# Performance work log

Hardware: AMD Instinct MI355X
Metric: run time of the kernel (lower is better)

## Reference

```python
import jax, jax.numpy as jnp
import numpy as np
from jax import lax

B, T_ENCO, N_INP, N_HID, T_DECO = 1024, 128, 128, 256, 24


def _lin(x, W, b):
    return x @ W.T + b


def _lstm_cell(x, h, c, Wih, Whh, bih, bhh):
    # PyTorch LSTMCell gate order: input, forget, cell(g), output
    g = x @ Wih.T + bih + h @ Whh.T + bhh
    i, f, gg, o = jnp.split(g, 4, axis=-1)
    c2 = jax.nn.sigmoid(f) * c + jax.nn.sigmoid(i) * jnp.tanh(gg)
    return jax.nn.sigmoid(o) * jnp.tanh(c2), c2


def setup_inputs() -> dict:
    key = jax.random.key(0)
    ks = iter(jax.random.split(key, 48))
    def w(shape, s=0.05):
        return jax.random.normal(next(ks), shape, jnp.float32) * s
    m = N_HID
    return {
        "input_p_q": jax.random.normal(next(ks), (B, T_ENCO, N_INP), jnp.float32),
        "label_p": jax.random.normal(next(ks), (B, T_DECO), jnp.float32),
        "Ue_W": w((m, T_ENCO)), "Ue_b": w((m,)),
        "Ue2_W": w((m, N_INP)), "Ue2_b": w((m,)),
        "We_W": w((m, 2 * N_HID)), "We_b": w((m,)),
        "Ve_W": w((1, m)), "Ve_b": w((1,)),
        "Ud_W": w((N_HID, N_HID)), "Ud_b": w((N_HID,)),
        "Wd_W": w((N_HID, 2 * N_HID)), "Wd_b": w((N_HID,)),
        "Vd_W": w((1, N_HID)), "Vd_b": w((1,)),
        "enc_Wih": w((4 * N_HID, N_INP)), "enc_Whh": w((4 * N_HID, N_HID)),
        "enc_bih": w((4 * N_HID,)), "enc_bhh": w((4 * N_HID,)),
        "mid_Wih": w((4 * N_HID, N_HID)), "mid_Whh": w((4 * N_HID, N_HID)),
        "mid_bih": w((4 * N_HID,)), "mid_bhh": w((4 * N_HID,)),
        "dec_Wih": w((4 * N_HID, N_HID)), "dec_Whh": w((4 * N_HID, N_HID)),
        "dec_bih": w((4 * N_HID,)), "dec_bhh": w((4 * N_HID,)),
        "reg_W": w((1, N_HID)), "reg_b": w((1,)),
    }


def reference(input_p_q, label_p, Ue_W, Ue_b, Ue2_W, Ue2_b, We_W, We_b, Ve_W, Ve_b,
              Ud_W, Ud_b, Wd_W, Wd_b, Vd_W, Vd_b,
              enc_Wih, enc_Whh, enc_bih, enc_bhh,
              mid_Wih, mid_Whh, mid_bih, mid_bhh,
              dec_Wih, dec_Whh, dec_bih, dec_bhh,
              reg_W, reg_b):
    bsz = input_p_q.shape[0]
    inputs = input_p_q[:, :T_ENCO, :]                       # [B, T, n_inp]
    # Ue(inputs.transpose(1,2)) is loop-invariant: [B, n_inp, m]
    ue_x = _lin(jnp.swapaxes(inputs, 1, 2), Ue_W, Ue_b)
    z = jnp.zeros((bsz, N_HID), inputs.dtype)

    # --- spatial-attention encoder (LSTMCell over time) ---
    def enc_step(carry, x_i):                               # x_i: [B, n_inp]
        h, c = carry
        hc = _lin(jnp.concatenate([h, c], axis=1), We_W, We_b)[:, None, :]
        xi = _lin(x_i, Ue2_W, Ue2_b)[:, None, :]
        score = _lin(jnp.tanh(hc + ue_x + xi), Ve_W, Ve_b)[..., 0]  # [B, n_inp]
        a = jax.nn.softmax(score, axis=1)
        h2, c2 = _lstm_cell(x_i * a, h, c, enc_Wih, enc_Whh, enc_bih, enc_bhh)
        return (h2, c2), h2

    _, enc_hs = lax.scan(enc_step, (z, z), jnp.swapaxes(inputs, 0, 1))  # [T, B, H]

    # --- middle single-layer LSTM (zero init state) ---
    def mid_step(carry, x_t):
        h, c = carry
        h2, c2 = _lstm_cell(x_t, h, c, mid_Wih, mid_Whh, mid_bih, mid_bhh)
        return (h2, c2), h2

    _, mid = lax.scan(mid_step, (z, z), enc_hs)
    mid = jnp.swapaxes(mid, 0, 1)                            # [B, T, H]
    ud_mid = _lin(mid, Ud_W, Ud_b)                           # loop-invariant

    # --- temporal-attention decoder (note: raw (un-softmaxed) scores used in bmm,
    #     matching the original code) ---
    def dec_step(carry, _):
        hi, ci = carry
        wd = _lin(jnp.concatenate([hi, ci], axis=1), Wd_W, Wd_b)[:, None, :]
        t = _lin(jnp.tanh(wd + ud_mid), Vd_W, Vd_b)[..., 0]  # [B, T]
        dec_in = jnp.einsum('bt,bth->bh', t, mid)
        hi2, ci2 = _lstm_cell(dec_in, hi, ci, dec_Wih, dec_Whh, dec_bih, dec_bhh)
        return (hi2, ci2), hi2

    _, dec = lax.scan(dec_step, (z, z), None, length=T_DECO + 6)
    dec = jnp.swapaxes(dec, 0, 1)                            # [B, T_deco+6, H]
    out = _lin(dec, reg_W, reg_b)[..., 0]                    # [B, T_deco+6]
    return out[:, -T_DECO:]
```

## Files before the change

kernel.cpp:

```cpp
#include <hip/hip_runtime.h>


#define B_   1024
#define T_   128
#define NI_  128
#define H_   256
#define H4_  1024
#define TD_  24
#define DS_  30
#define BB   4
#define TB   1024

typedef _Float16 hf_t;
typedef _Float16 half8  __attribute__((ext_vector_type(8)));
typedef _Float16 half2v __attribute__((ext_vector_type(2)));

__device__ __forceinline__ float sigm(float x) {
    return __builtin_amdgcn_rcpf(1.0f + __expf(-x));
}
__device__ __forceinline__ float tanh_f(float x) {
    float e = __expf(2.0f * x);
    return 1.0f - 2.0f * __builtin_amdgcn_rcpf(e + 1.0f);
}
__device__ __forceinline__ float fdot2f(half2v a, half2v b, float c) {
#if __has_builtin(__builtin_amdgcn_fdot2)
    return __builtin_amdgcn_fdot2(a, b, c, false);
#else
    return fmaf((float)a.x, (float)b.x, fmaf((float)a.y, (float)b.y, c));
#endif
}
__device__ __forceinline__ float dot8h(half8 w, half8 x, float acc) {
    acc = fdot2f(__builtin_shufflevector(w, w, 0, 1), __builtin_shufflevector(x, x, 0, 1), acc);
    acc = fdot2f(__builtin_shufflevector(w, w, 2, 3), __builtin_shufflevector(x, x, 2, 3), acc);
    acc = fdot2f(__builtin_shufflevector(w, w, 4, 5), __builtin_shufflevector(x, x, 4, 5), acc);
    acc = fdot2f(__builtin_shufflevector(w, w, 6, 7), __builtin_shufflevector(x, x, 6, 7), acc);
    return acc;
}
__device__ __forceinline__ hf_t nt_load_h(const hf_t* p) {
#if __has_builtin(__builtin_nontemporal_load)
    return __builtin_nontemporal_load(p);
#else
    return *p;
#endif
}
__device__ __forceinline__ void nt_store_h(hf_t v, hf_t* p) {
#if __has_builtin(__builtin_nontemporal_store)
    __builtin_nontemporal_store(v, p);
#else
    *p = v;
#endif
}

#define W_WE    0u
#define W_UE2   131072u
#define W_EWIH  163840u
#define W_EWHH  294912u
#define W_MWIH  557056u
#define W_MWHH  819200u
#define W_DWIH  1081344u
#define W_DWHH  1343488u
#define W_WD    1605632u
#define W_UD    1736704u
#define SCR_A   2097152u
#define SCR_B   35651584u

__global__ void convw_kernel(const float* __restrict__ sWE, const float* __restrict__ sUE2,
                             const float* __restrict__ sEI, const float* __restrict__ sEH,
                             const float* __restrict__ sMI, const float* __restrict__ sMH,
                             const float* __restrict__ sDI, const float* __restrict__ sDH,
                             const float* __restrict__ sWD, const float* __restrict__ sUD,
                             hf_t* __restrict__ dst) {
    const int gtid = blockIdx.x * blockDim.x + threadIdx.x;
    const int gs   = gridDim.x * blockDim.x;
    for (int n = gtid; n < 131072; n += gs) {
        int e = n & 7, q = n >> 3, k = q & 255, c = q >> 8, kq = c >> 4, i = c & 15;
        dst[W_WE + n] = (hf_t)sWE[k * 512 + kq * 128 + i * 8 + e];
    }
    for (int n = gtid; n < 32768; n += gs) {
        int e = n & 7, q = n >> 3, k = q & 255, c = q >> 8, kq = c >> 2, i = c & 3;
        dst[W_UE2 + n] = (hf_t)sUE2[k * 128 + kq * 32 + i * 8 + e];
    }
    for (int n = gtid; n < 131072; n += gs) {
        int e = n & 7, q = n >> 3, o = q & 1023, i = q >> 10;
        dst[W_EWIH + n] = (hf_t)sEI[o * 128 + i * 8 + e];
    }
    for (int n = gtid; n < 262144; n += gs) {
        int e = n & 7, q = n >> 3, o = q & 1023, i = q >> 10;
        int s = o * 256 + i * 8 + e;
        dst[W_EWHH + n] = (hf_t)sEH[s];
        dst[W_MWIH + n] = (hf_t)sMI[s];
        dst[W_MWHH + n] = (hf_t)sMH[s];
        dst[W_DWIH + n] = (hf_t)sDI[s];
        dst[W_DWHH + n] = (hf_t)sDH[s];
    }
    for (int n = gtid; n < 131072; n += gs) {
        int e = n & 7, q = n >> 3, k = q & 255, c = q >> 8, kq = c >> 4, i = c & 15;
        dst[W_WD + n] = (hf_t)sWD[k * 512 + kq * 128 + i * 8 + e];
    }
    for (int n = gtid; n < 65536; n += gs)
        dst[W_UD + n] = (hf_t)sUD[n];
}

#define O_HC    0
#define O_CF    1024
#define O_HM    2048
#define O_CMF   2560
#define O_XRAW  3584
#define O_XH    4096
#define O_XG    4352
#define O_HCXI  4608
#define O_SPART 5632
#define O_SBUF  6656
#define O_GBUF  7168
#define O_DINH  11264
#define O_HF    11776
#define O_VES   12800
#define O_VDS   13056

__global__ __launch_bounds__(TB, 4) void dsrnn_kernel(
    const float* __restrict__ inp,
    const float* __restrict__ UeW,  const float* __restrict__ Ueb,
    const float* __restrict__ Ue2b,
    const float* __restrict__ Web,
    const float* __restrict__ VeW,  const float* __restrict__ Veb,
    const float* __restrict__ Udb,
    const float* __restrict__ Wdb,
    const float* __restrict__ VdW,  const float* __restrict__ Vdb,
    const float* __restrict__ ebih, const float* __restrict__ ebhh,
    const float* __restrict__ mbih, const float* __restrict__ mbhh,
    const float* __restrict__ dbih, const float* __restrict__ dbhh,
    const float* __restrict__ rW,   const float* __restrict__ rb,
    const hf_t* __restrict__ wb,
    hf_t* __restrict__ scrA,
    hf_t* __restrict__ scrB,
    float* __restrict__ out)
{
    __shared__ float sm[16384];
    const int tid = threadIdx.x;
    const int b0  = blockIdx.x * BB;

    hf_t*  hc   = (hf_t*)(sm + O_HC);
    float* cf   = sm + O_CF;
    hf_t*  hm   = (hf_t*)(sm + O_HM);
    float* cmf  = sm + O_CMF;
    float* xraw = sm + O_XRAW;
    hf_t*  xh   = (hf_t*)(sm + O_XH);
    hf_t*  xg   = (hf_t*)(sm + O_XG);
    float* hcxi = sm + O_HCXI;
    float* spart= sm + O_SPART;
    float* sbuf = sm + O_SBUF;
    float* gbuf = sm + O_GBUF;
    hf_t*  dinh = (hf_t*)(sm + O_DINH);
    float* hful = sm + O_HF;
    float* ves  = sm + O_VES;
    float* vds  = sm + O_VDS;

    {
        const int j = tid & 127, kq8 = tid >> 7;
        for (int b = 0; b < BB; ++b) {
            __syncthreads();
            const float* Xg = inp + (size_t)(b0 + b) * T_ * NI_;
            for (int i = tid; i < T_ * NI_; i += TB) sm[i] = Xg[i];
            __syncthreads();
            hf_t* ub = scrA + (size_t)(b0 + b) * H_ * NI_;
            for (int k = kq8 * 32; k < kq8 * 32 + 32; ++k) {
                const float* wrow = UeW + (size_t)k * T_;
                float acc = Ueb[k];
#pragma unroll 4
                for (int t = 0; t < T_; ++t) acc = fmaf(wrow[t], sm[t * NI_ + j], acc);
                nt_store_h((hf_t)acc, ub + (size_t)k * NI_ + j);
            }
        }
    }
    __syncthreads();
    for (int i = tid; i < 3584; i += TB) sm[i] = 0.0f;
    if (tid < 256) { ves[tid] = VeW[tid]; vds[tid] = VdW[tid]; }
    __syncthreads();

    for (int t = 0; t < T_; ++t) {
        if (tid < 512) {
            const int b = tid >> 7, j = tid & 127;
            float v = inp[((size_t)(b0 + b) * T_ + t) * NI_ + j];
            xraw[b * NI_ + j] = v;
            xh[b * NI_ + j]   = (hf_t)v;
        }
        __syncthreads();

        {
            const int k = tid & 255, kq = tid >> 8;
            const half8* wWE = (const half8*)(wb + W_WE)  + (size_t)(kq * 16) * 256 + k;
            const half8* wU2 = (const half8*)(wb + W_UE2) + (size_t)(kq * 4)  * 256 + k;
            float a0 = 0.f, a1 = 0.f, a2 = 0.f, a3 = 0.f;
#pragma unroll 8
            for (int i = 0; i < 16; ++i) {
                half8 w = wWE[(size_t)i * 256];
                a0 = dot8h(w, *(const half8*)&hc[0 * 512 + kq * 128 + i * 8], a0);
                a1 = dot8h(w, *(const half8*)&hc[1 * 512 + kq * 128 + i * 8], a1);
                a2 = dot8h(w, *(const half8*)&hc[2 * 512 + kq * 128 + i * 8], a2);
                a3 = dot8h(w, *(const half8*)&hc[3 * 512 + kq * 128 + i * 8], a3);
            }
#pragma unroll
            for (int i = 0; i < 4; ++i) {
                half8 w = wU2[(size_t)i * 256];
                a0 = dot8h(w, *(const half8*)&xh[0 * 128 + kq * 32 + i * 8], a0);
                a1 = dot8h(w, *(const half8*)&xh[1 * 128 + kq * 32 + i * 8], a1);
                a2 = dot8h(w, *(const half8*)&xh[2 * 128 + kq * 32 + i * 8], a2);
                a3 = dot8h(w, *(const half8*)&xh[3 * 128 + kq * 32 + i * 8], a3);
            }
            gbuf[kq * 1024 + 0 * 256 + k] = a0;
            gbuf[kq * 1024 + 1 * 256 + k] = a1;
            gbuf[kq * 1024 + 2 * 256 + k] = a2;
            gbuf[kq * 1024 + 3 * 256 + k] = a3;
        }
        __syncthreads();
        {
            const int b = tid >> 8, k = tid & 255;
            hcxi[b * 256 + k] = gbuf[b * 256 + k] + gbuf[1024 + b * 256 + k]
                              + gbuf[2048 + b * 256 + k] + gbuf[3072 + b * 256 + k]
                              + Web[k] + Ue2b[k];
        }
        __syncthreads();

        {
            const int b = tid >> 8, r = tid & 255, kh = r >> 7, j = r & 127;
            const hf_t* up = scrA + ((size_t)(b0 + b) * 256 + kh * 128) * 128 + j;
            const float* hx = hcxi + b * 256 + kh * 128;
            const float* vw = ves + kh * 128;
            float acc = kh ? 0.f : Veb[0];
#pragma unroll 8
            for (int k2 = 0; k2 < 128; ++k2) {
                float u = (float)nt_load_h(up + (size_t)k2 * 128);
                acc = fmaf(vw[k2], tanh_f(hx[k2] + u), acc);
            }
            spart[tid] = acc;
        }
        __syncthreads();

        if (tid < 256) {
            const int b = tid >> 6, lane = tid & 63;
            const int base = b << 8;
            float sA = spart[base + lane]      + spart[base + 128 + lane];
            float sB = spart[base + 64 + lane] + spart[base + 192 + lane];
            float m = fmaxf(sA, sB);
            for (int d = 1; d < 64; d <<= 1) m = fmaxf(m, __shfl_xor(m, d));
            float eA = __expf(sA - m), eB = __expf(sB - m);
            float ssum = eA + eB;
            for (int d = 1; d < 64; d <<= 1) ssum += __shfl_xor(ssum, d);
            float inv = 1.0f / ssum;
            xg[b * NI_ + lane]      = (hf_t)(xraw[b * NI_ + lane] * eA * inv);
            xg[b * NI_ + lane + 64] = (hf_t)(xraw[b * NI_ + lane + 64] * eB * inv);
        }
        __syncthreads();

        {
            const int o = tid;
            const half8* wih = (const half8*)(wb + W_EWIH) + o;
            const half8* whh = (const half8*)(wb + W_EWHH) + o;
            float bias = ebih[o] + ebhh[o];
            float a0 = bias, a1 = bias, a2 = bias, a3 = bias;
#pragma unroll 8
            for (int i = 0; i < 16; ++i) {
                half8 w = wih[(size_t)i * 1024];
                a0 = dot8h(w, *(const half8*)&xg[0 * 128 + i * 8], a0);
                a1 = dot8h(w, *(const half8*)&xg[1 * 128 + i * 8], a1);
                a2 = dot8h(w, *(const half8*)&xg[2 * 128 + i * 8], a2);
                a3 = dot8h(w, *(const half8*)&xg[3 * 128 + i * 8], a3);
            }
#pragma unroll 8
            for (int i = 0; i < 32; ++i) {
                half8 w = whh[(size_t)i * 1024];
                a0 = dot8h(w, *(const half8*)&hc[0 * 512 + i * 8], a0);
                a1 = dot8h(w, *(const half8*)&hc[1 * 512 + i * 8], a1);
                a2 = dot8h(w, *(const half8*)&hc[2 * 512 + i * 8], a2);
                a3 = dot8h(w, *(const half8*)&hc[3 * 512 + i * 8], a3);
            }
            gbuf[0 * 1024 + o] = a0; gbuf[1 * 1024 + o] = a1;
            gbuf[2 * 1024 + o] = a2; gbuf[3 * 1024 + o] = a3;
        }
        __syncthreads();

        {
            const int b = tid >> 8, k = tid & 255;
            float gi = gbuf[b * H4_ + k];
            float gf = gbuf[b * H4_ + H_ + k];
            float gg = gbuf[b * H4_ + 2 * H_ + k];
            float go = gbuf[b * H4_ + 3 * H_ + k];
            float c2 = sigm(gf) * cf[b * H_ + k] + sigm(gi) * tanh_f(gg);
            float h2 = sigm(go) * tanh_f(c2);
            cf[b * H_ + k] = c2;
            hc[b * 512 + k]       = (hf_t)h2;
            hc[b * 512 + 256 + k] = (hf_t)c2;
        }
        __syncthreads();

        {
            const int o = tid;
            const half8* wih = (const half8*)(wb + W_MWIH) + o;
            const half8* whh = (const half8*)(wb + W_MWHH) + o;
            float bias = mbih[o] + mbhh[o];
            float a0 = bias, a1 = bias, a2 = bias, a3 = bias;
#pragma unroll 8
            for (int i = 0; i < 32; ++i) {
                half8 w = wih[(size_t)i * 1024];
                a0 = dot8h(w, *(const half8*)&hc[0 * 512 + i * 8], a0);
                a1 = dot8h(w, *(const half8*)&hc[1 * 512 + i * 8], a1);
                a2 = dot8h(w, *(const half8*)&hc[2 * 512 + i * 8], a2);
                a3 = dot8h(w, *(const half8*)&hc[3 * 512 + i * 8], a3);
            }
#pragma unroll 8
            for (int i = 0; i < 32; ++i) {
                half8 w = whh[(size_t)i * 1024];
                a0 = dot8h(w, *(const half8*)&hm[0 * 256 + i * 8], a0);
                a1 = dot8h(w, *(const half8*)&hm[1 * 256 + i * 8], a1);
                a2 = dot8h(w, *(const half8*)&hm[2 * 256 + i * 8], a2);
                a3 = dot8h(w, *(const half8*)&hm[3 * 256 + i * 8], a3);
            }
            gbuf[0 * 1024 + o] = a0; gbuf[1 * 1024 + o] = a1;
            gbuf[2 * 1024 + o] = a2; gbuf[3 * 1024 + o] = a3;
        }
        __syncthreads();

        {
            const int b = tid >> 8, k = tid & 255;
            float gi = gbuf[b * H4_ + k];
            float gf = gbuf[b * H4_ + H_ + k];
            float gg = gbuf[b * H4_ + 2 * H_ + k];
            float go = gbuf[b * H4_ + 3 * H_ + k];
            float c2 = sigm(gf) * cmf[b * H_ + k] + sigm(gi) * tanh_f(gg);
            float h2 = sigm(go) * tanh_f(c2);
            cmf[b * H_ + k] = c2;
            hm[b * 256 + k] = (hf_t)h2;
            scrB[((size_t)(b0 + b) * T_ + t) * H_ + k] = (hf_t)h2;
        }
        __syncthreads();
    }

    {
        const int b = tid >> 8, r = tid & 255, oh = r >> 7, tt = r & 127;
        const half8* mrow = (const half8*)(scrB + ((size_t)(b0 + b) * T_ + tt) * H_);
        half8 m[32];
#pragma unroll
        for (int i = 0; i < 32; ++i) m[i] = mrow[i];
        const half8* udw = (const half8*)(wb + W_UD);
        for (int o2 = 0; o2 < 128; ++o2) {
            const int o = oh * 128 + o2;
            const half8* ur = udw + (size_t)o * 32;
            float acc = Udb[o];
#pragma unroll 8
            for (int i = 0; i < 32; ++i) acc = dot8h(ur[i], m[i], acc);
            nt_store_h((hf_t)acc, scrA + ((size_t)(b0 + b) * 256 + o) * 128 + tt);
        }
    }
    __syncthreads();
    for (int i = tid; i < 2048; i += TB) sm[i] = 0.0f;
    __syncthreads();

    for (int s = 0; s < DS_; ++s) {
        {
            const int k = tid & 255, kq = tid >> 8;
            const half8* wWD = (const half8*)(wb + W_WD) + (size_t)(kq * 16) * 256 + k;
            float a0 = 0.f, a1 = 0.f, a2 = 0.f, a3 = 0.f;
#pragma unroll 8
            for (int i = 0; i < 16; ++i) {
                half8 w = wWD[(size_t)i * 256];
                a0 = dot8h(w, *(const half8*)&hc[0 * 512 + kq * 128 + i * 8], a0);
                a1 = dot8h(w, *(const half8*)&hc[1 * 512 + kq * 128 + i * 8], a1);
                a2 = dot8h(w, *(const half8*)&hc[2 * 512 + kq * 128 + i * 8], a2);
                a3 = dot8h(w, *(const half8*)&hc[3 * 512 + kq * 128 + i * 8], a3);
            }
            gbuf[kq * 1024 + 0 * 256 + k] = a0;
            gbuf[kq * 1024 + 1 * 256 + k] = a1;
            gbuf[kq * 1024 + 2 * 256 + k] = a2;
            gbuf[kq * 1024 + 3 * 256 + k] = a3;
        }
        __syncthreads();
        {
            const int b = tid >> 8, k = tid & 255;
            hcxi[b * 256 + k] = gbuf[b * 256 + k] + gbuf[1024 + b * 256 + k]
                              + gbuf[2048 + b * 256 + k] + gbuf[3072 + b * 256 + k]
                              + Wdb[k];
        }
        __syncthreads();

        {
            const int b = tid >> 8, r = tid & 255, kh = r >> 7, j = r & 127;
            const hf_t* up = scrA + ((size_t)(b0 + b) * 256 + kh * 128) * 128 + j;
            const float* hx = hcxi + b * 256 + kh * 128;
            const float* vw = vds + kh * 128;
            float acc = kh ? 0.f : Vdb[0];
#pragma unroll 8
            for (int k2 = 0; k2 < 128; ++k2) {
                float u = (float)nt_load_h(up + (size_t)k2 * 128);
                acc = fmaf(vw[k2], tanh_f(hx[k2] + u), acc);
            }
            spart[tid] = acc;
        }
        __syncthreads();
        if (tid < 512) {
            const int b = tid >> 7, j = tid & 127;
            sbuf[b * T_ + j] = spart[(b << 8) + j] + spart[(b << 8) + 128 + j];
        }
        __syncthreads();

        {
            const int b = tid >> 8, h = tid & 255;
            const hf_t* mp = scrB + (size_t)(b0 + b) * T_ * H_ + h;
            float acc = 0.0f;
            for (int j = 0; j < T_; ++j)
                acc = fmaf(sbuf[b * T_ + j], (float)mp[(size_t)j * H_], acc);
            dinh[b * 256 + h] = (hf_t)acc;
        }
        __syncthreads();

        {
            const int o = tid;
            const half8* wih = (const half8*)(wb + W_DWIH) + o;
            const half8* whh = (const half8*)(wb + W_DWHH) + o;
            float bias = dbih[o] + dbhh[o];
            float a0 = bias, a1 = bias, a2 = bias, a3 = bias;
#pragma unroll 8
            for (int i = 0; i < 32; ++i) {
                half8 w = wih[(size_t)i * 1024];
                a0 = dot8h(w, *(const half8*)&dinh[0 * 256 + i * 8], a0);
                a1 = dot8h(w, *(const half8*)&dinh[1 * 256 + i * 8], a1);
                a2 = dot8h(w, *(const half8*)&dinh[2 * 256 + i * 8], a2);
                a3 = dot8h(w, *(const half8*)&dinh[3 * 256 + i * 8], a3);
            }
#pragma unroll 8
            for (int i = 0; i < 32; ++i) {
                half8 w = whh[(size_t)i * 1024];
                a0 = dot8h(w, *(const half8*)&hc[0 * 512 + i * 8], a0);
                a1 = dot8h(w, *(const half8*)&hc[1 * 512 + i * 8], a1);
                a2 = dot8h(w, *(const half8*)&hc[2 * 512 + i * 8], a2);
                a3 = dot8h(w, *(const half8*)&hc[3 * 512 + i * 8], a3);
            }
            gbuf[0 * 1024 + o] = a0; gbuf[1 * 1024 + o] = a1;
            gbuf[2 * 1024 + o] = a2; gbuf[3 * 1024 + o] = a3;
        }
        __syncthreads();

        {
            const int b = tid >> 8, k = tid & 255;
            float gi = gbuf[b * H4_ + k];
            float gf = gbuf[b * H4_ + H_ + k];
            float gg = gbuf[b * H4_ + 2 * H_ + k];
            float go = gbuf[b * H4_ + 3 * H_ + k];
            float c2 = sigm(gf) * cf[b * H_ + k] + sigm(gi) * tanh_f(gg);
            float h2 = sigm(go) * tanh_f(c2);
            cf[b * H_ + k] = c2;
            hc[b * 512 + k]       = (hf_t)h2;
            hc[b * 512 + 256 + k] = (hf_t)c2;
            hful[b * H_ + k] = h2;
        }
        __syncthreads();

        if (s >= 6 && tid < 256) {
            const int b = tid >> 6, lane = tid & 63;
            float p = rW[lane]       * hful[b * H_ + lane]
                    + rW[lane + 64]  * hful[b * H_ + lane + 64]
                    + rW[lane + 128] * hful[b * H_ + lane + 128]
                    + rW[lane + 192] * hful[b * H_ + lane + 192];
            for (int d = 1; d < 64; d <<= 1) p += __shfl_xor(p, d);
            if (lane == 0) out[(size_t)(b0 + b) * TD_ + (s - 6)] = p + rb[0];
        }
        __syncthreads();
    }
}

extern "C" void kernel_launch(void* const* d_in, const int* in_sizes, int n_in,
                              void* d_out, int out_size, void* d_ws, size_t ws_size,
                              hipStream_t stream) {
    const float* inp  = (const float*)d_in[0];
    const float* UeW  = (const float*)d_in[2];
    const float* Ueb  = (const float*)d_in[3];
    const float* Ue2W = (const float*)d_in[4];
    const float* Ue2b = (const float*)d_in[5];
    const float* WeW  = (const float*)d_in[6];
    const float* Web  = (const float*)d_in[7];
    const float* VeW  = (const float*)d_in[8];
    const float* Veb  = (const float*)d_in[9];
    const float* UdW  = (const float*)d_in[10];
    const float* Udb  = (const float*)d_in[11];
    const float* WdW  = (const float*)d_in[12];
    const float* Wdb  = (const float*)d_in[13];
    const float* VdW  = (const float*)d_in[14];
    const float* Vdb  = (const float*)d_in[15];
    const float* eWih = (const float*)d_in[16];
    const float* eWhh = (const float*)d_in[17];
    const float* ebih = (const float*)d_in[18];
    const float* ebhh = (const float*)d_in[19];
    const float* mWih = (const float*)d_in[20];
    const float* mWhh = (const float*)d_in[21];
    const float* mbih = (const float*)d_in[22];
    const float* mbhh = (const float*)d_in[23];
    const float* dWih = (const float*)d_in[24];
    const float* dWhh = (const float*)d_in[25];
    const float* dbih = (const float*)d_in[26];
    const float* dbhh = (const float*)d_in[27];
    const float* rW   = (const float*)d_in[28];
    const float* rb   = (const float*)d_in[29];

    hf_t* wsb  = (hf_t*)d_ws;
    hf_t* scrA = wsb + SCR_A;
    hf_t* scrB = wsb + SCR_B;

    convw_kernel<<<512, 256, 0, stream>>>(WeW, Ue2W, eWih, eWhh, mWih, mWhh,
                                          dWih, dWhh, WdW, UdW, wsb);

    dsrnn_kernel<<<B_ / BB, TB, 0, stream>>>(
        inp, UeW, Ueb, Ue2b, Web, VeW, Veb, Udb, Wdb, VdW, Vdb,
        ebih, ebhh, mbih, mbhh, dbih, dbhh, rW, rb,
        wsb, scrA, scrB, (float*)d_out);
}
```

Baseline: 10.75 ms.

## Keep half of the Ue/Ud attention projections resident in enlarged dynamic LDS

Switches to 160KB of dynamic shared memory and keeps the first 128 rows of the precomputed Ue(x) and Ud(mid) projections per batch element in LDS, so half of the per-step attention reads no longer go to global scratch. The working buffers are compacted and aliased. The LSTM cell states move into registers, and the regression dot product is reduced with a warp shuffle plus a small LDS reduce. In exchange, LDS use grows far beyond the old 64KB, which limits blocks per CU to one. The Ue precompute is also reorganised into two half-width passes with extra syncs.

```diff
diff --git a/kernel.cpp b/kernel.cpp
--- a/kernel.cpp
+++ b/kernel.cpp
@@ -10,6 +10,7 @@
 #define DS_  30
 #define BB   4
 #define TB   1024
+#define LDS_BYTES 163840u
 
 typedef _Float16 hf_t;
 typedef _Float16 half8  __attribute__((ext_vector_type(8)));
@@ -102,20 +103,14 @@
 }
 
 #define O_HC    0
-#define O_CF    1024
-#define O_HM    2048
-#define O_CMF   2560
-#define O_XRAW  3584
-#define O_XH    4096
-#define O_XG    4352
-#define O_HCXI  4608
-#define O_SPART 5632
-#define O_SBUF  6656
-#define O_GBUF  7168
-#define O_DINH  11264
-#define O_HF    11776
-#define O_VES   12800
-#define O_VDS   13056
+#define O_HM    1024
+#define O_XRAW  1536
+#define O_XHG   2048
+#define O_HCXI  2304
+#define O_VES   3328
+#define O_VDS   3584
+#define O_RED   3840
+#define O_GBUF  4096
 
 __global__ __launch_bounds__(TB, 4) void dsrnn_kernel(
     const float* __restrict__ inp,
@@ -135,54 +130,64 @@
     hf_t* __restrict__ scrB,
     float* __restrict__ out)
 {
-    __shared__ float sm[16384];
+    extern __shared__ float sm[];
+    float* wk = sm;
+    hf_t*  u1 = (hf_t*)(sm + 8192);
+
     const int tid = threadIdx.x;
     const int b0  = blockIdx.x * BB;
 
-    hf_t*  hc   = (hf_t*)(sm + O_HC);
-    float* cf   = sm + O_CF;
-    hf_t*  hm   = (hf_t*)(sm + O_HM);
-    float* cmf  = sm + O_CMF;
-    float* xraw = sm + O_XRAW;
-    hf_t*  xh   = (hf_t*)(sm + O_XH);
-    hf_t*  xg   = (hf_t*)(sm + O_XG);
-    float* hcxi = sm + O_HCXI;
-    float* spart= sm + O_SPART;
-    float* sbuf = sm + O_SBUF;
-    float* gbuf = sm + O_GBUF;
-    hf_t*  dinh = (hf_t*)(sm + O_DINH);
-    float* hful = sm + O_HF;
-    float* ves  = sm + O_VES;
-    float* vds  = sm + O_VDS;
+    hf_t*  hc   = (hf_t*)(wk + O_HC);
+    hf_t*  hm   = (hf_t*)(wk + O_HM);
+    float* xraw = wk + O_XRAW;
+    hf_t*  xhg  = (hf_t*)(wk + O_XHG);
+    float* hcxi = wk + O_HCXI;
+    float* ves  = wk + O_VES;
+    float* vds  = wk + O_VDS;
+    float* red  = wk + O_RED;
+    float* gbuf = wk + O_GBUF;
+    hf_t*  dinh = (hf_t*)(wk + O_HM);
 
     {
-        const int j = tid & 127, kq8 = tid >> 7;
+        const int jj = tid & 63;
+        const int kg = tid >> 6;
         for (int b = 0; b < BB; ++b) {
-            __syncthreads();
             const float* Xg = inp + (size_t)(b0 + b) * T_ * NI_;
-            for (int i = tid; i < T_ * NI_; i += TB) sm[i] = Xg[i];
-            __syncthreads();
-            hf_t* ub = scrA + (size_t)(b0 + b) * H_ * NI_;
-            for (int k = kq8 * 32; k < kq8 * 32 + 32; ++k) {
-                const float* wrow = UeW + (size_t)k * T_;
-                float acc = Ueb[k];
+            for (int jh = 0; jh < 2; ++jh) {
+                __syncthreads();
+                for (int i = tid; i < 128 * 64; i += TB) {
+                    int t = i >> 6, j2 = i & 63;
+                    wk[i] = Xg[t * NI_ + jh * 64 + j2];
+                }
+                __syncthreads();
+                const int j = jh * 64 + jj;
+                for (int k = kg * 16; k < kg * 16 + 16; ++k) {
+                    const float* wrow = UeW + (size_t)k * T_;
+                    float acc = Ueb[k];
 #pragma unroll 4
-                for (int t = 0; t < T_; ++t) acc = fmaf(wrow[t], sm[t * NI_ + j], acc);
-                nt_store_h((hf_t)acc, ub + (size_t)k * NI_ + j);
+                    for (int t = 0; t < T_; ++t) acc = fmaf(wrow[t], wk[t * 64 + jj], acc);
+                    if (k < 128)
+                        u1[((size_t)(b * 128) + k) * 128 + j] = (hf_t)acc;
+                    else
+                        nt_store_h((hf_t)acc,
+                                   scrA + (((size_t)(b0 + b) * 128) + (k - 128)) * 128 + j);
+                }
             }
         }
     }
     __syncthreads();
-    for (int i = tid; i < 3584; i += TB) sm[i] = 0.0f;
+    for (int i = tid; i < 1536; i += TB) wk[i] = 0.0f;
     if (tid < 256) { ves[tid] = VeW[tid]; vds[tid] = VdW[tid]; }
     __syncthreads();
+
+    float c_enc = 0.0f, c_mid = 0.0f;
 
     for (int t = 0; t < T_; ++t) {
         if (tid < 512) {
             const int b = tid >> 7, j = tid & 127;
             float v = inp[((size_t)(b0 + b) * T_ + t) * NI_ + j];
             xraw[b * NI_ + j] = v;
-            xh[b * NI_ + j]   = (hf_t)v;
+            xhg[b * NI_ + j]  = (hf_t)v;
         }
         __syncthreads();
 
@@ -202,10 +207,10 @@
 #pragma unroll
             for (int i = 0; i < 4; ++i) {
                 half8 w = wU2[(size_t)i * 256];
-                a0 = dot8h(w, *(const half8*)&xh[0 * 128 + kq * 32 + i * 8], a0);
-                a1 = dot8h(w, *(const half8*)&xh[1 * 128 + kq * 32 + i * 8], a1);
-                a2 = dot8h(w, *(const half8*)&xh[2 * 128 + kq * 32 + i * 8], a2);
-                a3 = dot8h(w, *(const half8*)&xh[3 * 128 + kq * 32 + i * 8], a3);
+                a0 = dot8h(w, *(const half8*)&xhg[0 * 128 + kq * 32 + i * 8], a0);
+                a1 = dot8h(w, *(const half8*)&xhg[1 * 128 + kq * 32 + i * 8], a1);
+                a2 = dot8h(w, *(const half8*)&xhg[2 * 128 + kq * 32 + i * 8], a2);
+                a3 = dot8h(w, *(const half8*)&xhg[3 * 128 + kq * 32 + i * 8], a3);
             }
             gbuf[kq * 1024 + 0 * 256 + k] = a0;
             gbuf[kq * 1024 + 1 * 256 + k] = a1;
@@ -223,32 +228,41 @@
 
         {
             const int b = tid >> 8, r = tid & 255, kh = r >> 7, j = r & 127;
-            const hf_t* up = scrA + ((size_t)(b0 + b) * 256 + kh * 128) * 128 + j;
             const float* hx = hcxi + b * 256 + kh * 128;
             const float* vw = ves + kh * 128;
             float acc = kh ? 0.f : Veb[0];
-#pragma unroll 8
-            for (int k2 = 0; k2 < 128; ++k2) {
-                float u = (float)nt_load_h(up + (size_t)k2 * 128);
-                acc = fmaf(vw[k2], tanh_f(hx[k2] + u), acc);
-            }
-            spart[tid] = acc;
+            if (kh == 0) {
+                const hf_t* up = u1 + ((size_t)(b * 128)) * 128 + j;
+#pragma unroll 8
+                for (int k2 = 0; k2 < 128; ++k2) {
+                    float u = (float)up[(size_t)k2 * 128];
+                    acc = fmaf(vw[k2], tanh_f(hx[k2] + u), acc);
+                }
+            } else {
+                const hf_t* up = scrA + ((size_t)(b0 + b) * 128) * 128 + j;
+#pragma unroll 8
+                for (int k2 = 0; k2 < 128; ++k2) {
+                    float u = (float)nt_load_h(up + (size_t)k2 * 128);
+                    acc = fmaf(vw[k2], tanh_f(hx[k2] + u), acc);
+                }
+            }
+            gbuf[tid] = acc;
         }
         __syncthreads();
 
         if (tid < 256) {
             const int b = tid >> 6, lane = tid & 63;
             const int base = b << 8;
-            float sA = spart[base + lane]      + spart[base + 128 + lane];
-            float sB = spart[base + 64 + lane] + spart[base + 192 + lane];
+            float sA = gbuf[base + lane]      + gbuf[base + 128 + lane];
+            float sB = gbuf[base + 64 + lane] + gbuf[base + 192 + lane];
             float m = fmaxf(sA, sB);
             for (int d = 1; d < 64; d <<= 1) m = fmaxf(m, __shfl_xor(m, d));
             float eA = __expf(sA - m), eB = __expf(sB - m);
             float ssum = eA + eB;
             for (int d = 1; d < 64; d <<= 1) ssum += __shfl_xor(ssum, d);
             float inv = 1.0f / ssum;
-            xg[b * NI_ + lane]      = (hf_t)(xraw[b * NI_ + lane] * eA * inv);
-            xg[b * NI_ + lane + 64] = (hf_t)(xraw[b * NI_ + lane + 64] * eB * inv);
+            xhg[b * NI_ + lane]      = (hf_t)(xraw[b * NI_ + lane] * eA * inv);
+            xhg[b * NI_ + lane + 64] = (hf_t)(xraw[b * NI_ + lane + 64] * eB * inv);
         }
         __syncthreads();
 
@@ -261,10 +275,10 @@
 #pragma unroll 8
             for (int i = 0; i < 16; ++i) {
                 half8 w = wih[(size_t)i * 1024];
-                a0 = dot8h(w, *(const half8*)&xg[0 * 128 + i * 8], a0);
-                a1 = dot8h(w, *(const half8*)&xg[1 * 128 + i * 8], a1);
-                a2 = dot8h(w, *(const half8*)&xg[2 * 128 + i * 8], a2);
-                a3 = dot8h(w, *(const half8*)&xg[3 * 128 + i * 8], a3);
+                a0 = dot8h(w, *(const half8*)&xhg[0 * 128 + i * 8], a0);
+                a1 = dot8h(w, *(const half8*)&xhg[1 * 128 + i * 8], a1);
+                a2 = dot8h(w, *(const half8*)&xhg[2 * 128 + i * 8], a2);
+                a3 = dot8h(w, *(const half8*)&xhg[3 * 128 + i * 8], a3);
             }
 #pragma unroll 8
             for (int i = 0; i < 32; ++i) {
@@ -285,9 +299,9 @@
             float gf = gbuf[b * H4_ + H_ + k];
             float gg = gbuf[b * H4_ + 2 * H_ + k];
             float go = gbuf[b * H4_ + 3 * H_ + k];
-            float c2 = sigm(gf) * cf[b * H_ + k] + sigm(gi) * tanh_f(gg);
+            float c2 = sigm(gf) * c_enc + sigm(gi) * tanh_f(gg);
             float h2 = sigm(go) * tanh_f(c2);
-            cf[b * H_ + k] = c2;
+            c_enc = c2;
             hc[b * 512 + k]       = (hf_t)h2;
             hc[b * 512 + 256 + k] = (hf_t)c2;
         }
@@ -326,9 +340,9 @@
             float gf = gbuf[b * H4_ + H_ + k];
             float gg = gbuf[b * H4_ + 2 * H_ + k];
             float go = gbuf[b * H4_ + 3 * H_ + k];
-            float c2 = sigm(gf) * cmf[b * H_ + k] + sigm(gi) * tanh_f(gg);
+            float c2 = sigm(gf) * c_mid + sigm(gi) * tanh_f(gg);
             float h2 = sigm(go) * tanh_f(c2);
-            cmf[b * H_ + k] = c2;
+            c_mid = c2;
             hm[b * 256 + k] = (hf_t)h2;
             scrB[((size_t)(b0 + b) * T_ + t) * H_ + k] = (hf_t)h2;
         }
@@ -338,22 +352,25 @@
     {
         const int b = tid >> 8, r = tid & 255, oh = r >> 7, tt = r & 127;
         const half8* mrow = (const half8*)(scrB + ((size_t)(b0 + b) * T_ + tt) * H_);
-        half8 m[32];
-#pragma unroll
-        for (int i = 0; i < 32; ++i) m[i] = mrow[i];
         const half8* udw = (const half8*)(wb + W_UD);
         for (int o2 = 0; o2 < 128; ++o2) {
             const int o = oh * 128 + o2;
             const half8* ur = udw + (size_t)o * 32;
             float acc = Udb[o];
 #pragma unroll 8
-            for (int i = 0; i < 32; ++i) acc = dot8h(ur[i], m[i], acc);
-            nt_store_h((hf_t)acc, scrA + ((size_t)(b0 + b) * 256 + o) * 128 + tt);
+            for (int i = 0; i < 32; ++i) acc = dot8h(ur[i], mrow[i], acc);
+            if (oh == 0)
+                u1[((size_t)(b * 128) + o) * 128 + tt] = (hf_t)acc;
+            else
+                nt_store_h((hf_t)acc,
+                           scrA + (((size_t)(b0 + b) * 128) + o2) * 128 + tt);
         }
     }
     __syncthreads();
-    for (int i = tid; i < 2048; i += TB) sm[i] = 0.0f;
+    for (int i = tid; i < 1024; i += TB) wk[i] = 0.0f;
     __syncthreads();
+
+    float c_dec = 0.0f;
 
     for (int s = 0; s < DS_; ++s) {
         {
@@ -384,30 +401,40 @@
 
         {
             const int b = tid >> 8, r = tid & 255, kh = r >> 7, j = r & 127;
-            const hf_t* up = scrA + ((size_t)(b0 + b) * 256 + kh * 128) * 128 + j;
             const float* hx = hcxi + b * 256 + kh * 128;
             const float* vw = vds + kh * 128;
             float acc = kh ? 0.f : Vdb[0];
-#pragma unroll 8
-            for (int k2 = 0; k2 < 128; ++k2) {
-                float u = (float)nt_load_h(up + (size_t)k2 * 128);
-                acc = fmaf(vw[k2], tanh_f(hx[k2] + u), acc);
-            }
-            spart[tid] = acc;
+            if (kh == 0) {
+                const hf_t* up = u1 + ((size_t)(b * 128)) * 128 + j;
+#pragma unroll 8
+                for (int k2 = 0; k2 < 128; ++k2) {
+                    float u = (float)up[(size_t)k2 * 128];
+                    acc = fmaf(vw[k2], tanh_f(hx[k2] + u), acc);
+                }
+            } else {
+                const hf_t* up = scrA + ((size_t)(b0 + b) * 128) * 128 + j;
+#pragma unroll 8
+                for (int k2 = 0; k2 < 128; ++k2) {
+                    float u = (float)nt_load_h(up + (size_t)k2 * 128);
+                    acc = fmaf(vw[k2], tanh_f(hx[k2] + u), acc);
+                }
+            }
+            gbuf[tid] = acc;
         }
         __syncthreads();
         if (tid < 512) {
             const int b = tid >> 7, j = tid & 127;
-            sbuf[b * T_ + j] = spart[(b << 8) + j] + spart[(b << 8) + 128 + j];
+            gbuf[1024 + b * 128 + j] = gbuf[(b << 8) + j] + gbuf[(b << 8) + 128 + j];
         }
         __syncthreads();
 
         {
             const int b = tid >> 8, h = tid & 255;
             const hf_t* mp = scrB + (size_t)(b0 + b) * T_ * H_ + h;
+            const float* sb = gbuf + 1024 + b * 128;
             float acc = 0.0f;
             for (int j = 0; j < T_; ++j)
-                acc = fmaf(sbuf[b * T_ + j], (float)mp[(size_t)j * H_], acc);
+                acc = fmaf(sb[j], (float)mp[(size_t)j * H_], acc);
             dinh[b * 256 + h] = (hf_t)acc;
         }
         __syncthreads();
@@ -439,29 +466,32 @@
         }
         __syncthreads();
 
+        float h2dec;
         {
             const int b = tid >> 8, k = tid & 255;
             float gi = gbuf[b * H4_ + k];
             float gf = gbuf[b * H4_ + H_ + k];
             float gg = gbuf[b * H4_ + 2 * H_ + k];
             float go = gbuf[b * H4_ + 3 * H_ + k];
-            float c2 = sigm(gf) * cf[b * H_ + k] + sigm(gi) * tanh_f(gg);
-            float h2 = sigm(go) * tanh_f(c2);
-            cf[b * H_ + k] = c2;
-            hc[b * 512 + k]       = (hf_t)h2;
+            float c2 = sigm(gf) * c_dec + sigm(gi) * tanh_f(gg);
+            h2dec = sigm(go) * tanh_f(c2);
+            c_dec = c2;
+            hc[b * 512 + k]       = (hf_t)h2dec;
             hc[b * 512 + 256 + k] = (hf_t)c2;
-            hful[b * H_ + k] = h2;
-        }
-        __syncthreads();
-
-        if (s >= 6 && tid < 256) {
-            const int b = tid >> 6, lane = tid & 63;
-            float p = rW[lane]       * hful[b * H_ + lane]
-                    + rW[lane + 64]  * hful[b * H_ + lane + 64]
-                    + rW[lane + 128] * hful[b * H_ + lane + 128]
-                    + rW[lane + 192] * hful[b * H_ + lane + 192];
+        }
+        __syncthreads();
+
+        if (s >= 6) {
+            const int k = tid & 255;
+            float p = rW[k] * h2dec;
             for (int d = 1; d < 64; d <<= 1) p += __shfl_xor(p, d);
-            if (lane == 0) out[(size_t)(b0 + b) * TD_ + (s - 6)] = p + rb[0];
+            if ((tid & 63) == 0) red[tid >> 6] = p;
+        }
+        __syncthreads();
+        if (s >= 6 && tid < 4) {
+            float v = red[tid * 4] + red[tid * 4 + 1]
+                    + red[tid * 4 + 2] + red[tid * 4 + 3] + rb[0];
+            out[(size_t)(b0 + tid) * TD_ + (s - 6)] = v;
         }
         __syncthreads();
     }
@@ -504,10 +534,17 @@
     hf_t* scrA = wsb + SCR_A;
     hf_t* scrB = wsb + SCR_B;
 
+    static bool attr_set = false;
+    if (!attr_set) {
+        hipFuncSetAttribute((const void*)dsrnn_kernel,
+                            hipFuncAttributeMaxDynamicSharedMemorySize, LDS_BYTES);
+        attr_set = true;
+    }
+
     convw_kernel<<<512, 256, 0, stream>>>(WeW, Ue2W, eWih, eWhh, mWih, mWhh,
                                           dWih, dWhh, WdW, UdW, wsb);
 
-    dsrnn_kernel<<<B_ / BB, TB, 0, stream>>>(
+    dsrnn_kernel<<<B_ / BB, TB, LDS_BYTES, stream>>>(
         inp, UeW, Ueb, Ue2b, Web, VeW, Veb, Udb, Wdb, VdW, Vdb,
         ebih, ebhh, mbih, mbhh, dbih, dbhh, rW, rb,
         wsb, scrA, scrB, (float*)d_out);
```

New measurement: 10.31 ms. 1.04x faster.
